# Optimization experiments

Hardware: AMD Instinct MI355X
Metric: run time of the kernel (lower is better)

## Reference

```python
import jax, jax.numpy as jnp
import numpy as np

M_CACHE, N_MODEL, D_HEAD = 8192, 4096, 128
H_HEADS = N_MODEL // D_HEAD  # 32
SEQ_LEN = 16


def setup_inputs() -> dict:
    key = jax.random.key(0)
    ks = jax.random.split(key, 6)
    X = jax.random.normal(ks[0], (SEQ_LEN, N_MODEL), dtype=jnp.float32)
    W_q = jax.random.normal(ks[1], (N_MODEL, N_MODEL), dtype=jnp.float32) * 0.02
    W_k = jax.random.normal(ks[2], (N_MODEL, N_MODEL), dtype=jnp.float32) * 0.02
    W_v = jax.random.normal(ks[3], (N_MODEL, N_MODEL), dtype=jnp.float32) * 0.02
    cache_K = jax.random.normal(ks[4], (H_HEADS, M_CACHE, D_HEAD), dtype=jnp.float32)
    cache_V = jax.random.normal(ks[5], (H_HEADS, M_CACHE, D_HEAD), dtype=jnp.float32)
    return {"X": X, "W_q": W_q, "W_k": W_k, "W_v": W_v,
            "cache_K": cache_K, "cache_V": cache_V, "P": 4096}


def reference(X, W_q, W_k, W_v, cache_K, cache_V, P):
    S = X.shape[0]
    H, M, D = cache_K.shape
    # QKV projections, split into heads: [S, N] -> [H, S, D]
    q = (X @ W_q).reshape(S, H, D).transpose(1, 0, 2)
    k = (X @ W_k).reshape(S, H, D).transpose(1, 0, 2)
    v = (X @ W_v).reshape(S, H, D).transpose(1, 0, 2)
    # KV-cache slice write at position P
    cK = cache_K.at[:, P:P + S, :].set(k)
    cV = cache_V.at[:, P:P + S, :].set(v)
    # Unscaled attention over the FULL cache length (faithful to original)
    scores = jnp.einsum('hsd,hmd->hsm', q, cK)          # [H, S, M]
    weights = jax.nn.softmax(scores, axis=-1)
    out = jnp.einsum('hsm,hmd->hsd', weights, cV)        # [H, S, D]
    # Original does .view(S, H*D) on the [H, S, D] tensor (no transpose)
    return out.reshape(S, H * D)
```

## Files before the change

kernel.cpp:

```cpp
#include <hip/hip_runtime.h>

#define S_LEN 16
#define NMODEL 4096
#define DHEAD 128
#define HHEADS 32
#define MCACHE 8192
#define SPLITK 32
#define KSLICE (NMODEL / SPLITK)
#define CHUNK_W 64
#define NCHT (MCACHE / CHUNK_W)
#define SPAD 20

#define PART_ELEMS   ((size_t)3 * SPLITK * S_LEN * NMODEL)
#define OPART_USH    ((size_t)HHEADS * NCHT * S_LEN * DHEAD)
#define OPART_FLOATS (OPART_USH / 2)
#define REGION_ELEMS (PART_ELEMS > OPART_FLOATS ? PART_ELEMS : OPART_FLOATS)
#define STAT_ELEMS   ((size_t)HHEADS * NCHT * S_LEN)

typedef _Float16 half8 __attribute__((ext_vector_type(8)));
typedef float    f32x4 __attribute__((ext_vector_type(4)));

__device__ __forceinline__ half8 cvt8(float4 a, float4 b) {
    half8 h;
    h[0] = (_Float16)a.x; h[1] = (_Float16)a.y; h[2] = (_Float16)a.z; h[3] = (_Float16)a.w;
    h[4] = (_Float16)b.x; h[5] = (_Float16)b.y; h[6] = (_Float16)b.z; h[7] = (_Float16)b.w;
    return h;
}
__device__ __forceinline__ unsigned short f2h(float f) {
    _Float16 h = (_Float16)f; unsigned short u; __builtin_memcpy(&u, &h, 2); return u;
}
__device__ __forceinline__ float h2f(unsigned short u) {
    _Float16 h; __builtin_memcpy(&h, &u, 2); return (float)h;
}

__global__ __launch_bounds__(256) void qkv_gemm(const float* __restrict__ X,
                                                const float* __restrict__ Wq,
                                                const float* __restrict__ Wk,
                                                const float* __restrict__ Wv,
                                                float* __restrict__ part) {
    const int tid   = threadIdx.x;
    const int col2  = blockIdx.x * 256 + tid;
    const int split = blockIdx.y;
    const int mat   = blockIdx.z;
    const float* __restrict__ W = (mat == 0) ? Wq : (mat == 1) ? Wk : Wv;
    const int k0 = split * KSLICE;

    __shared__ float Xs[KSLICE][S_LEN];
    for (int i = tid; i < KSLICE * S_LEN; i += 256) {
        const int s = i & 15, k = i >> 4;
        Xs[k][s] = X[s * NMODEL + k0 + k];
    }
    __syncthreads();

    float2 acc[S_LEN];
#pragma unroll
    for (int s = 0; s < S_LEN; ++s) { acc[s].x = 0.f; acc[s].y = 0.f; }

    const float2* __restrict__ Wp = (const float2*)(W + (size_t)k0 * NMODEL) + col2;

#pragma unroll 8
    for (int k = 0; k < KSLICE; ++k) {
        const float2 w = Wp[(size_t)k * (NMODEL / 2)];
        const float4* __restrict__ xr = (const float4*)&Xs[k][0];
#pragma unroll
        for (int s4 = 0; s4 < 4; ++s4) {
            const float4 xv = xr[s4];
            acc[s4 * 4 + 0].x += xv.x * w.x;  acc[s4 * 4 + 0].y += xv.x * w.y;
            acc[s4 * 4 + 1].x += xv.y * w.x;  acc[s4 * 4 + 1].y += xv.y * w.y;
            acc[s4 * 4 + 2].x += xv.z * w.x;  acc[s4 * 4 + 2].y += xv.z * w.y;
            acc[s4 * 4 + 3].x += xv.w * w.x;  acc[s4 * 4 + 3].y += xv.w * w.y;
        }
    }

    float2* __restrict__ pp =
        (float2*)(part + (size_t)(mat * SPLITK + split) * S_LEN * NMODEL) + col2;
#pragma unroll
    for (int s = 0; s < S_LEN; ++s) pp[(size_t)s * (NMODEL / 2)] = acc[s];
}

__global__ __launch_bounds__(256) void qkv_reduce(const float* __restrict__ part,
                                                  float* __restrict__ qkv) {
    const int i4   = blockIdx.x * 256 + threadIdx.x;
    const int flat = i4 * 4;
    const int mat  = flat / (S_LEN * NMODEL);
    const int rem  = flat % (S_LEN * NMODEL);
    float4 sum = {0.f, 0.f, 0.f, 0.f};
#pragma unroll 8
    for (int sp = 0; sp < SPLITK; ++sp) {
        const float4 v = *(const float4*)(part +
            (size_t)(mat * SPLITK + sp) * (S_LEN * NMODEL) + rem);
        sum.x += v.x; sum.y += v.y; sum.z += v.z; sum.w += v.w;
    }
    *(float4*)(qkv + flat) = sum;
}

__global__ __launch_bounds__(128) void attn_partial(const float* __restrict__ qkv,
                                                    const float* __restrict__ cacheK,
                                                    const float* __restrict__ cacheV,
                                                    const int* __restrict__ Pp,
                                                    unsigned short* __restrict__ opart,
                                                    float* __restrict__ mstat,
                                                    float* __restrict__ lstat) {
    const int bx   = blockIdx.x;
    const int h    = blockIdx.y;
    const int tid  = threadIdx.x;
    const int wv   = tid >> 6;
    const int lane = tid & 63;
    const int c    = bx * 2 + wv;
    const int c0   = c * CHUNK_W;
    const int P    = *Pp;
    const int lo   = (P > c0) ? P : c0;
    const int hi_  = (P + S_LEN < c0 + CHUNK_W) ? (P + S_LEN) : (c0 + CHUNK_W);
    const bool overlap = (lo < hi_);

    const float* qb = qkv;
    const float* kb = qkv + S_LEN * NMODEL;
    const float* vb = qkv + 2 * S_LEN * NMODEL;

    __shared__ float sct[2][CHUNK_W][SPAD];
    __shared__ float ml[2][S_LEN], ll[2][S_LEN];

    const int row16 = lane & 15;
    const int kg    = lane >> 4;

    {
        half8 qf[4];
#pragma unroll
        for (int cs = 0; cs < 4; ++cs) {
            const float* qr = qb + row16 * NMODEL + h * DHEAD + cs * 32 + kg * 8;
            qf[cs] = cvt8(*(const float4*)qr, *(const float4*)(qr + 4));
        }
#pragma unroll
        for (int t = 0; t < 4; ++t) {
            const float* krow = cacheK +
                ((size_t)h * MCACHE + c0 + t * 16 + row16) * DHEAD + kg * 8;
            f32x4 acc = {0.f, 0.f, 0.f, 0.f};
#pragma unroll
            for (int cs = 0; cs < 4; ++cs) {
                const float4 ka = *(const float4*)(krow + cs * 32);
                const float4 kc = *(const float4*)(krow + cs * 32 + 4);
                acc = __builtin_amdgcn_mfma_f32_16x16x32_f16(qf[cs], cvt8(ka, kc),
                                                             acc, 0, 0, 0);
            }
            *(float4*)&sct[wv][t * 16 + row16][kg * 4] = *(float4*)&acc;
        }

        if (overlap) {
            const int sq = kg, dsl = row16, doff = dsl * 8;
            float4 q0[4], q1[4];
#pragma unroll
            for (int j = 0; j < 4; ++j) {
                const int s = sq * 4 + j;
                q0[j] = *(const float4*)(qb + s * NMODEL + h * DHEAD + doff);
                q1[j] = *(const float4*)(qb + s * NMODEL + h * DHEAD + doff + 4);
            }
            for (int gm = lo; gm < hi_; ++gm) {
                const float* kr = kb + (size_t)(gm - P) * NMODEL + h * DHEAD + doff;
                const float4 ka = *(const float4*)(kr);
                const float4 kc = *(const float4*)(kr + 4);
                float pr[4];
#pragma unroll
                for (int j = 0; j < 4; ++j) {
                    pr[j] = ka.x * q0[j].x + ka.y * q0[j].y + ka.z * q0[j].z + ka.w * q0[j].w
                          + kc.x * q1[j].x + kc.y * q1[j].y + kc.z * q1[j].z + kc.w * q1[j].w;
                }
#pragma unroll
                for (int j = 0; j < 4; ++j) {
                    float v = pr[j];
                    v += __shfl_xor(v, 1, 64);
                    v += __shfl_xor(v, 2, 64);
                    v += __shfl_xor(v, 4, 64);
                    v += __shfl_xor(v, 8, 64);
                    pr[j] = v;
                }
                if (dsl == 0) {
                    float4 w; w.x = pr[0]; w.y = pr[1]; w.z = pr[2]; w.w = pr[3];
                    *(float4*)&sct[wv][gm - c0][sq * 4] = w;
                }
            }
        }
    }
    __syncthreads();

    {
        for (int s = 0; s < S_LEN; ++s) {
            const float v = sct[wv][lane][s];
            float mx = v;
            for (int off = 32; off > 0; off >>= 1) mx = fmaxf(mx, __shfl_xor(mx, off, 64));
            const float e = __expf(v - mx);
            sct[wv][lane][s] = e;
            float sum = e;
            for (int off = 32; off > 0; off >>= 1) sum += __shfl_xor(sum, off, 64);
            if (lane == 0) { ml[wv][s] = mx; ll[wv][s] = sum; }
        }
    }
    __syncthreads();

    {
        const int sq = lane >> 4, dsl = lane & 15, doff = dsl * 8;
        const float* vbase = cacheV + ((size_t)h * MCACHE + c0) * DHEAD + doff;
        float a[4][8];
#pragma unroll
        for (int j = 0; j < 4; ++j)
#pragma unroll
            for (int k = 0; k < 8; ++k) a[j][k] = 0.f;

        for (int m = 0; m < CHUNK_W; ++m) {
            const float4 p4 = *(const float4*)&sct[wv][m][sq * 4];
            const float4 v0 = *(const float4*)(vbase + (size_t)m * DHEAD);
            const float4 v1 = *(const float4*)(vbase + (size_t)m * DHEAD + 4);
            const float pj[4] = {p4.x, p4.y, p4.z, p4.w};
#pragma unroll
            for (int j = 0; j < 4; ++j) {
                a[j][0] += pj[j] * v0.x; a[j][1] += pj[j] * v0.y;
                a[j][2] += pj[j] * v0.z; a[j][3] += pj[j] * v0.w;
                a[j][4] += pj[j] * v1.x; a[j][5] += pj[j] * v1.y;
                a[j][6] += pj[j] * v1.z; a[j][7] += pj[j] * v1.w;
            }
        }

        if (overlap) {
            for (int gm = lo; gm < hi_; ++gm) {
                const float4 p4 = *(const float4*)&sct[wv][gm - c0][sq * 4];
                const float* vn = vb + (size_t)(gm - P) * NMODEL + h * DHEAD + doff;
                const float* vo = cacheV + ((size_t)h * MCACHE + gm) * DHEAD + doff;
                const float4 n0 = *(const float4*)(vn);
                const float4 n1 = *(const float4*)(vn + 4);
                const float4 o0 = *(const float4*)(vo);
                const float4 o1 = *(const float4*)(vo + 4);
                const float pj[4] = {p4.x, p4.y, p4.z, p4.w};
#pragma unroll
                for (int j = 0; j < 4; ++j) {
                    a[j][0] += pj[j] * (n0.x - o0.x); a[j][1] += pj[j] * (n0.y - o0.y);
                    a[j][2] += pj[j] * (n0.z - o0.z); a[j][3] += pj[j] * (n0.w - o0.w);
                    a[j][4] += pj[j] * (n1.x - o1.x); a[j][5] += pj[j] * (n1.y - o1.y);
                    a[j][6] += pj[j] * (n1.z - o1.z); a[j][7] += pj[j] * (n1.w - o1.w);
                }
            }
        }

        const size_t ob = ((size_t)h * NCHT + c) * S_LEN * DHEAD;
#pragma unroll
        for (int j = 0; j < 4; ++j) {
            const int s = sq * 4 + j;
            uint4 pk;
            unsigned short* us = (unsigned short*)&pk;
#pragma unroll
            for (int k = 0; k < 8; ++k) us[k] = f2h(a[j][k]);
            *(uint4*)&opart[ob + (size_t)s * DHEAD + doff] = pk;
        }
    }

    if (tid < 32) {
        const int w2 = tid >> 4, s = tid & 15;
        const int cc = bx * 2 + w2;
        mstat[((size_t)h * S_LEN + s) * NCHT + cc] = ml[w2][s];
        lstat[((size_t)h * S_LEN + s) * NCHT + cc] = ll[w2][s];
    }
}

__global__ __launch_bounds__(512) void attn_combine(const unsigned short* __restrict__ opart,
                                                    const float* __restrict__ mstat,
                                                    const float* __restrict__ lstat,
                                                    float* __restrict__ out) {
    const int tid = threadIdx.x;
    const int cg  = tid >> 7;
    const int d   = tid & 127;
    const int s   = blockIdx.x;
    const int h   = blockIdx.y;

    __shared__ float mlds[NCHT], llds[NCHT], wlds[NCHT];
    __shared__ float olds[4][DHEAD];
    __shared__ float Llds[4];

    const size_t sb = ((size_t)h * S_LEN + s) * NCHT;
    if (tid < NCHT) { mlds[tid] = mstat[sb + tid]; llds[tid] = lstat[sb + tid]; }
    __syncthreads();

    float gmax = fmaxf(mlds[tid & 63], mlds[(tid & 63) + 64]);
    for (int off = 32; off > 0; off >>= 1) gmax = fmaxf(gmax, __shfl_xor(gmax, off, 64));

    if (tid < NCHT) wlds[tid] = __expf(mlds[tid] - gmax);
    __syncthreads();

    float o = 0.f, L = 0.f;
    for (int c = cg; c < NCHT; c += 4) {
        const float w = wlds[c];
        o += w * h2f(opart[(((size_t)h * NCHT + c) * S_LEN + s) * DHEAD + d]);
        L += w * llds[c];
    }
    olds[cg][d] = o;
    if (d == 0) Llds[cg] = L;
    __syncthreads();

    if (tid < DHEAD) {
        const float ot = olds[0][tid] + olds[1][tid] + olds[2][tid] + olds[3][tid];
        const float Lt = Llds[0] + Llds[1] + Llds[2] + Llds[3];
        out[((size_t)h * S_LEN + s) * DHEAD + tid] = ot / Lt;
    }
}

extern "C" void kernel_launch(void* const* d_in, const int* in_sizes, int n_in,
                              void* d_out, int out_size, void* d_ws, size_t ws_size,
                              hipStream_t stream) {
    const float* X      = (const float*)d_in[0];
    const float* Wq     = (const float*)d_in[1];
    const float* Wk     = (const float*)d_in[2];
    const float* Wv     = (const float*)d_in[3];
    const float* cacheK = (const float*)d_in[4];
    const float* cacheV = (const float*)d_in[5];
    const int*   P      = (const int*)d_in[6];
    float* out = (float*)d_out;
    float* ws  = (float*)d_ws;

    float*          qkv   = ws;
    float*          part  = qkv + 3 * S_LEN * NMODEL;
    unsigned short* opart = (unsigned short*)part;
    float*          mstat = part + REGION_ELEMS;
    float*          lstat = mstat + STAT_ELEMS;

    qkv_gemm<<<dim3(8, SPLITK, 3), 256, 0, stream>>>(X, Wq, Wk, Wv, part);
    qkv_reduce<<<(3 * S_LEN * NMODEL / 4) / 256, 256, 0, stream>>>(part, qkv);
    attn_partial<<<dim3(NCHT / 2, HHEADS), 128, 0, stream>>>(qkv, cacheK, cacheV, P,
                                                             opart, mstat, lstat);
    attn_combine<<<dim3(S_LEN, HHEADS), 512, 0, stream>>>(opart, mstat, lstat, out);
}
```

Baseline: 150.8 us.

## Use MFMA for P·V in attention chunk kernel with transposed score layout

Replaces the scalar FMA accumulation of softmax weights times the V cache with 16x16x32 f16 MFMA instructions. The shared score buffer is transposed to [S][M] with padding so A-fragments can be read as contiguous rows. V is now loaded as scalar per-element strided reads converted to f16, which may hurt coalescing relative to the previous float4 loads. The probabilities are also rounded to f16, adding some precision loss.

```diff
diff --git a/kernel.cpp b/kernel.cpp
--- a/kernel.cpp
+++ b/kernel.cpp
@@ -9,7 +9,7 @@
 #define KSLICE (NMODEL / SPLITK)
 #define CHUNK_W 64
 #define NCHT (MCACHE / CHUNK_W)
-#define SPAD 20
+#define MPAD 68
 
 #define PART_ELEMS   ((size_t)3 * SPLITK * S_LEN * NMODEL)
 #define OPART_USH    ((size_t)HHEADS * NCHT * S_LEN * DHEAD)
@@ -117,7 +117,7 @@
     const float* kb = qkv + S_LEN * NMODEL;
     const float* vb = qkv + 2 * S_LEN * NMODEL;
 
-    __shared__ float sct[2][CHUNK_W][SPAD];
+    __shared__ float scs[2][S_LEN][MPAD];
     __shared__ float ml[2][S_LEN], ll[2][S_LEN];
 
     const int row16 = lane & 15;
@@ -142,7 +142,9 @@
                 acc = __builtin_amdgcn_mfma_f32_16x16x32_f16(qf[cs], cvt8(ka, kc),
                                                              acc, 0, 0, 0);
             }
-            *(float4*)&sct[wv][t * 16 + row16][kg * 4] = *(float4*)&acc;
+#pragma unroll
+            for (int r = 0; r < 4; ++r)
+                scs[wv][kg * 4 + r][t * 16 + row16] = acc[r];
         }
 
         if (overlap) {
@@ -174,8 +176,9 @@
                     pr[j] = v;
                 }
                 if (dsl == 0) {
-                    float4 w; w.x = pr[0]; w.y = pr[1]; w.z = pr[2]; w.w = pr[3];
-                    *(float4*)&sct[wv][gm - c0][sq * 4] = w;
+#pragma unroll
+                    for (int j = 0; j < 4; ++j)
+                        scs[wv][sq * 4 + j][gm - c0] = pr[j];
                 }
             }
         }
@@ -184,11 +187,11 @@
 
     {
         for (int s = 0; s < S_LEN; ++s) {
-            const float v = sct[wv][lane][s];
+            const float v = scs[wv][s][lane];
             float mx = v;
             for (int off = 32; off > 0; off >>= 1) mx = fmaxf(mx, __shfl_xor(mx, off, 64));
             const float e = __expf(v - mx);
-            sct[wv][lane][s] = e;
+            scs[wv][s][lane] = e;
             float sum = e;
             for (int off = 32; off > 0; off >>= 1) sum += __shfl_xor(sum, off, 64);
             if (lane == 0) { ml[wv][s] = mx; ll[wv][s] = sum; }
@@ -197,57 +200,41 @@
     __syncthreads();
 
     {
-        const int sq = lane >> 4, dsl = lane & 15, doff = dsl * 8;
-        const float* vbase = cacheV + ((size_t)h * MCACHE + c0) * DHEAD + doff;
-        float a[4][8];
-#pragma unroll
-        for (int j = 0; j < 4; ++j)
-#pragma unroll
-            for (int k = 0; k < 8; ++k) a[j][k] = 0.f;
-
-        for (int m = 0; m < CHUNK_W; ++m) {
-            const float4 p4 = *(const float4*)&sct[wv][m][sq * 4];
-            const float4 v0 = *(const float4*)(vbase + (size_t)m * DHEAD);
-            const float4 v1 = *(const float4*)(vbase + (size_t)m * DHEAD + 4);
-            const float pj[4] = {p4.x, p4.y, p4.z, p4.w};
-#pragma unroll
-            for (int j = 0; j < 4; ++j) {
-                a[j][0] += pj[j] * v0.x; a[j][1] += pj[j] * v0.y;
-                a[j][2] += pj[j] * v0.z; a[j][3] += pj[j] * v0.w;
-                a[j][4] += pj[j] * v1.x; a[j][5] += pj[j] * v1.y;
-                a[j][6] += pj[j] * v1.z; a[j][7] += pj[j] * v1.w;
-            }
-        }
-
-        if (overlap) {
-            for (int gm = lo; gm < hi_; ++gm) {
-                const float4 p4 = *(const float4*)&sct[wv][gm - c0][sq * 4];
-                const float* vn = vb + (size_t)(gm - P) * NMODEL + h * DHEAD + doff;
-                const float* vo = cacheV + ((size_t)h * MCACHE + gm) * DHEAD + doff;
-                const float4 n0 = *(const float4*)(vn);
-                const float4 n1 = *(const float4*)(vn + 4);
-                const float4 o0 = *(const float4*)(vo);
-                const float4 o1 = *(const float4*)(vo + 4);
-                const float pj[4] = {p4.x, p4.y, p4.z, p4.w};
-#pragma unroll
-                for (int j = 0; j < 4; ++j) {
-                    a[j][0] += pj[j] * (n0.x - o0.x); a[j][1] += pj[j] * (n0.y - o0.y);
-                    a[j][2] += pj[j] * (n0.z - o0.z); a[j][3] += pj[j] * (n0.w - o0.w);
-                    a[j][4] += pj[j] * (n1.x - o1.x); a[j][5] += pj[j] * (n1.y - o1.y);
-                    a[j][6] += pj[j] * (n1.z - o1.z); a[j][7] += pj[j] * (n1.w - o1.w);
+        half8 af[2];
+#pragma unroll
+        for (int ks = 0; ks < 2; ++ks) {
+            const float4 pa = *(const float4*)&scs[wv][row16][ks * 32 + kg * 8];
+            const float4 pb = *(const float4*)&scs[wv][row16][ks * 32 + kg * 8 + 4];
+            af[ks] = cvt8(pa, pb);
+        }
+        const float* vball = cacheV + ((size_t)h * MCACHE + c0) * DHEAD;
+        const size_t obase = ((size_t)h * NCHT + c) * S_LEN * DHEAD;
+
+#pragma unroll
+        for (int dt = 0; dt < 8; ++dt) {
+            const int dcol = dt * 16 + row16;
+            f32x4 acc = {0.f, 0.f, 0.f, 0.f};
+#pragma unroll
+            for (int ks = 0; ks < 2; ++ks) {
+                half8 bf;
+#pragma unroll
+                for (int j = 0; j < 8; ++j)
+                    bf[j] = (_Float16)vball[(size_t)(ks * 32 + kg * 8 + j) * DHEAD + dcol];
+                acc = __builtin_amdgcn_mfma_f32_16x16x32_f16(af[ks], bf, acc, 0, 0, 0);
+            }
+            if (overlap) {
+                for (int gm = lo; gm < hi_; ++gm) {
+                    const float vn = vb[(size_t)(gm - P) * NMODEL + h * DHEAD + dcol];
+                    const float vo = cacheV[((size_t)h * MCACHE + gm) * DHEAD + dcol];
+                    const float dv = vn - vo;
+#pragma unroll
+                    for (int r = 0; r < 4; ++r)
+                        acc[r] += scs[wv][kg * 4 + r][gm - c0] * dv;
                 }
             }
-        }
-
-        const size_t ob = ((size_t)h * NCHT + c) * S_LEN * DHEAD;
-#pragma unroll
-        for (int j = 0; j < 4; ++j) {
-            const int s = sq * 4 + j;
-            uint4 pk;
-            unsigned short* us = (unsigned short*)&pk;
-#pragma unroll
-            for (int k = 0; k < 8; ++k) us[k] = f2h(a[j][k]);
-            *(uint4*)&opart[ob + (size_t)s * DHEAD + doff] = pk;
+#pragma unroll
+            for (int r = 0; r < 4; ++r)
+                opart[obase + (size_t)(kg * 4 + r) * DHEAD + dcol] = f2h(acc[r]);
         }
     }
 
```

New measurement: 167.8 us. 11.2% more time.
